# Kernel tuning notes

Measured on AMD Instinct MI355X. Metric: run time of the kernel, lower is better.

The kernel has to match this reference:

```python
import jax, jax.numpy as jnp
import numpy as np

B, V, CODE_NUM = 64, 100, 4096
CODE_SIZE, ATT, VISIT, TIME, HID, OUT = 256, 128, 256, 64, 512, 90
TYPE_NUM = 32
NEG = -2.0 ** 31


def setup_inputs() -> dict:
    key = jax.random.key(0)
    ks = jax.random.split(key, 24)
    s = 0.02
    return {
        'code_x': jax.random.randint(ks[0], (B, V, CODE_NUM), 0, 2).astype(jnp.float32),
        'code_type0': jax.random.randint(ks[1], (CODE_NUM + 1,), 0, TYPE_NUM),
        'code_type1': jax.random.randint(ks[2], (CODE_NUM + 1,), 0, TYPE_NUM),
        'code_type2': jax.random.randint(ks[3], (CODE_NUM + 1,), 0, TYPE_NUM),
        'lens': jax.random.randint(ks[4], (B,), 1, V + 1),
        'intervals': jax.random.uniform(ks[5], (B, V), dtype=jnp.float32),
        # encoder: code + 3 type embedding tables (rows 1..code_num used)
        'code_emb': jax.random.normal(ks[6], (CODE_NUM + 1, CODE_SIZE), jnp.float32) * s,
        't0_emb': jax.random.normal(ks[7], (TYPE_NUM, CODE_SIZE), jnp.float32) * s,
        't1_emb': jax.random.normal(ks[8], (TYPE_NUM, CODE_SIZE), jnp.float32) * s,
        't2_emb': jax.random.normal(ks[9], (TYPE_NUM, CODE_SIZE), jnp.float32) * s,
        # visit self-attention (no bias, per nn.Linear(..., bias=False))
        'Wq': jax.random.normal(ks[10], (CODE_SIZE, ATT), jnp.float32) * s,
        'Wk': jax.random.normal(ks[11], (CODE_SIZE, ATT), jnp.float32) * s,
        'Wv': jax.random.normal(ks[12], (CODE_SIZE, VISIT), jnp.float32) * s,
        # time embedding Linear(1, time_size)
        'time_w': jax.random.normal(ks[13], (TIME,), jnp.float32) * s,
        'time_b': jnp.zeros((TIME,), jnp.float32),
        # GRUCell params (torch layout: gates ordered r,z,n)
        'gru_Wih': jax.random.normal(ks[14], (3 * HID, VISIT + TIME), jnp.float32) * s,
        'gru_Whh': jax.random.normal(ks[15], (3 * HID, HID), jnp.float32) * s,
        'gru_bih': jnp.zeros((3 * HID,), jnp.float32),
        'gru_bhh': jnp.zeros((3 * HID,), jnp.float32),
        # classifier
        'cls_W': jax.random.normal(ks[16], (OUT, HID), jnp.float32) * s,
        'cls_b': jnp.zeros((OUT,), jnp.float32),
    }


def reference(code_x, code_type0, code_type1, code_type2, lens, intervals,
              code_emb, t0_emb, t1_emb, t2_emb, Wq, Wk, Wv, time_w, time_b,
              gru_Wih, gru_Whh, gru_bih, gru_bhh, cls_W, cls_b):
    # --- Encoder (vectorized): multi-hot slot i corresponds to code id i+1 ---
    E = (code_emb[1:]
         + t0_emb[code_type0[1:]]
         + t1_emb[code_type1[1:]]
         + t2_emb[code_type2[1:]])                      # [CODE_NUM, CODE_SIZE]
    active = (code_x > 0).astype(E.dtype)               # [B, V, CODE_NUM]
    counts = jnp.maximum(active.sum(-1, keepdims=True), 1.0)
    v_emb_ini = jnp.einsum('bvc,cd->bvd', active, E) / counts  # mean over codes
    visit_mask = jnp.arange(V)[None, :] < lens[:, None]        # [B, V]
    v_emb_ini = v_emb_ini * visit_mask[..., None]              # padded visits stay 0

    # --- Context-aware visit self-attention ---
    Q = v_emb_ini @ Wq                                   # [B, V, ATT]
    K = v_emb_ini @ Wk
    Vv = v_emb_ini @ Wv                                  # [B, V, VISIT]
    alpha = jnp.einsum('bqa,bka->bqk', Q, K)
    alpha = jnp.where(visit_mask[:, None, :], alpha, NEG)  # mask keys
    alpha = jax.nn.softmax(alpha, axis=2)
    v_emb = jnp.einsum('bqk,bkd->bqd', alpha, Vv) + Vv     # [B, V, VISIT]

    # --- Time-aware input ---
    t_emb = intervals[..., None] * time_w + time_b         # [B, V, TIME]
    x = jnp.concatenate([v_emb, t_emb], axis=-1)           # [B, V, VISIT+TIME]

    # --- GRU over visits, gated by per-patient length ---
    def step(h, xm):
        xt, mt = xm                                        # xt [B,D], mt [B]
        gi = xt @ gru_Wih.T + gru_bih
        gh = h @ gru_Whh.T + gru_bhh
        ir, iz, inn = jnp.split(gi, 3, axis=-1)
        hr, hz, hn = jnp.split(gh, 3, axis=-1)
        r = jax.nn.sigmoid(ir + hr)
        z = jax.nn.sigmoid(iz + hz)
        n = jnp.tanh(inn + r * hn)
        h_new = (1.0 - z) * n + z * h
        h = jnp.where(mt[:, None], h_new, h)
        return h, None

    h0 = jnp.zeros((B, HID), x.dtype)
    h_final, _ = jax.lax.scan(step, h0, (x.transpose(1, 0, 2), visit_mask.T))

    # --- Classifier (dropout p=0 -> identity) ---
    return jax.nn.sigmoid(h_final @ cls_W.T + cls_b)       # [B, OUT]
```

## Files before the change

kernel.cpp:

```cpp
#include <hip/hip_runtime.h>
#include <hip/hip_bf16.h>

typedef float  f32x4 __attribute__((ext_vector_type(4)));
typedef short  s16x8 __attribute__((ext_vector_type(8)));

#define NEGBIG -1e30f

__device__ __forceinline__ unsigned short f2b(float f) {
    union { float f; unsigned u; } c; c.f = f;
    unsigned r = c.u + 0x7FFF + ((c.u >> 16) & 1);
    return (unsigned short)(r >> 16);
}
__device__ __forceinline__ float b2f(unsigned short h) {
    union { unsigned u; float f; } c; c.u = ((unsigned)h) << 16;
    return c.f;
}
__device__ __forceinline__ float sigm(float x) { return 1.f / (1.f + __expf(-x)); }

__device__ __forceinline__ s16x8 ld_b128_sc(const unsigned short* p) {
    s16x8 r;
    asm volatile("global_load_dwordx4 %0, %1, off sc0 sc1" : "=v"(r) : "v"(p));
    return r;
}
__device__ __forceinline__ void st_short_sc(unsigned short* p, unsigned short v) {
    unsigned int dv = v;
    asm volatile("global_store_short %0, %1, off sc0 sc1" :: "v"(p), "v"(dv) : "memory");
}
__device__ __forceinline__ void st_dword_sc(float* p, float v) {
    asm volatile("global_store_dword %0, %1, off sc0 sc1" :: "v"(p), "v"(v) : "memory");
}

__global__ void init_zero(int* flags, unsigned short* hb0) {
    int t = threadIdx.x;
    for (int i = t; i < 1024; i += 256) flags[i] = 0;
    for (int i = t; i < 32768; i += 256) hb0[i] = 0;
}

__global__ void prep_w(const float* Wq, const float* Wk, const float* Wv,
                       const float* gWih, const float* gWhh,
                       unsigned short* wcat, unsigned short* wih, unsigned short* whh) {
    int idx = blockIdx.x * 256 + threadIdx.x;
    int stride = gridDim.x * 256;
    const int N1 = 131072, N2 = 491520, N3 = 786432;
    for (; idx < N1 + N2 + N3; idx += stride) {
        if (idx < N1) {
            int n = idx >> 8, k = idx & 255;
            float v;
            if (n < 128) v = Wq[k * 128 + n];
            else if (n < 256) v = Wk[k * 128 + (n - 128)];
            else v = Wv[k * 256 + (n - 256)];
            wcat[n * 256 + k] = f2b(v);
        } else if (idx < N1 + N2) {
            int i = idx - N1; wih[i] = f2b(gWih[i]);
        } else {
            int i = idx - N1 - N2; whh[i] = f2b(gWhh[i]);
        }
    }
}

__global__ __launch_bounds__(256) void prep_et(const float* code_emb, const int* ct0, const int* ct1, const int* ct2,
                                               const float* t0e, const float* t1e, const float* t2e,
                                               unsigned short* ET) {
    __shared__ float tile[64][65];
    const int d0 = blockIdx.x * 64, c0 = blockIdx.y * 64;
    const int t = threadIdx.x;
    for (int p = 0; p < 16; ++p) {
        int idx = p * 256 + t;
        int dl = idx & 63, cl = idx >> 6;
        int code = c0 + cl + 1;
        int d = d0 + dl;
        float v = code_emb[code * 256 + d] + t0e[ct0[code] * 256 + d]
                + t1e[ct1[code] * 256 + d] + t2e[ct2[code] * 256 + d];
        tile[dl][cl] = v;
    }
    __syncthreads();
    for (int p = 0; p < 2; ++p) {
        int idx = p * 256 + t;
        int dl = idx >> 3, ch = idx & 7;
        s16x8 pk;
#pragma unroll
        for (int e = 0; e < 8; ++e) pk[e] = (short)f2b(tile[dl][ch * 8 + e]);
        *(s16x8*)(ET + (size_t)(d0 + dl) * 4096 + c0 + ch * 8) = pk;
    }
}

__global__ __launch_bounds__(256) void enc_gemm(const float* code_x, const unsigned short* ET,
                                                const int* lens, unsigned short* Vb) {
    __shared__ __align__(16) char sm[4096 + 32768 + 128];
    char* As = sm;
    char* Bs = sm + 4096;
    float* cl = (float*)(sm + 4096 + 32768);
    const int m0 = blockIdx.x * 32;
    const int t = threadIdx.x, l = t & 63, w = t >> 6;
    const int lr = l & 15, lq = l >> 4, l7 = l & 7;
    const int sr = t >> 3, sc = t & 7;
    f32x4 acc[2][4];
#pragma unroll
    for (int a = 0; a < 2; ++a)
#pragma unroll
        for (int b = 0; b < 4; ++b) acc[a][b] = (f32x4){0.f, 0.f, 0.f, 0.f};
    int cnt = 0;
    for (int it = 0; it < 64; ++it) {
        const int k0 = it * 64;
        const float* ga = code_x + (size_t)(m0 + sr) * 4096 + k0 + sc * 8;
        f32x4 a0 = *(const f32x4*)ga;
        f32x4 a1 = *(const f32x4*)(ga + 4);
        s16x8 ap;
#pragma unroll
        for (int e = 0; e < 4; ++e) { bool on = a0[e] > 0.f; ap[e] = on ? (short)0x3F80 : (short)0; cnt += on ? 1 : 0; }
#pragma unroll
        for (int e = 0; e < 4; ++e) { bool on = a1[e] > 0.f; ap[4 + e] = on ? (short)0x3F80 : (short)0; cnt += on ? 1 : 0; }
        *(s16x8*)(As + sr * 128 + ((sc ^ (sr & 7)) << 4)) = ap;
#pragma unroll
        for (int rd = 0; rd < 8; ++rd) {
            int i = rd * 256 + t;
            int n = i >> 3, cc = i & 7;
            s16x8 bv = *(const s16x8*)(ET + (size_t)n * 4096 + k0 + cc * 8);
            *(s16x8*)(Bs + n * 128 + ((cc ^ (n & 7)) << 4)) = bv;
        }
        __syncthreads();
#pragma unroll
        for (int kk = 0; kk < 2; ++kk) {
            const int cp = kk * 4 + lq;
            s16x8 af[2], bf[4];
#pragma unroll
            for (int mt = 0; mt < 2; ++mt)
                af[mt] = *(const s16x8*)(As + (mt * 16 + lr) * 128 + ((cp ^ l7) << 4));
#pragma unroll
            for (int nt = 0; nt < 4; ++nt)
                bf[nt] = *(const s16x8*)(Bs + ((w * 4 + nt) * 16 + lr) * 128 + ((cp ^ l7) << 4));
#pragma unroll
            for (int mt = 0; mt < 2; ++mt)
#pragma unroll
                for (int nt = 0; nt < 4; ++nt)
                    acc[mt][nt] = __builtin_amdgcn_mfma_f32_16x16x32_bf16(af[mt], bf[nt], acc[mt][nt], 0, 0, 0);
        }
        __syncthreads();
    }
    float fc = (float)cnt;
    fc += __shfl_xor(fc, 1); fc += __shfl_xor(fc, 2); fc += __shfl_xor(fc, 4);
    if (sc == 0) cl[sr] = fmaxf(fc, 1.f);
    __syncthreads();
#pragma unroll
    for (int mt = 0; mt < 2; ++mt)
#pragma unroll
        for (int i = 0; i < 4; ++i) {
            int m = mt * 16 + lq * 4 + i;
            int gm = m0 + m;
            float rc = 1.f / cl[m];
            unsigned bi = (unsigned)gm / 100u;
            unsigned vi = (unsigned)gm - bi * 100u;
            float msk = ((int)vi < lens[bi]) ? 1.f : 0.f;
#pragma unroll
            for (int nt = 0; nt < 4; ++nt) {
                int n = (w * 4 + nt) * 16 + lr;
                Vb[(size_t)gm * 256 + n] = f2b(acc[mt][nt][i] * rc * msk);
            }
        }
}

__global__ __launch_bounds__(256) void gemm_bf16(const unsigned short* A, const unsigned short* Bm,
                                                 int K, int Ntot, int mode,
                                                 unsigned short* outp, const float* bias) {
    __shared__ __align__(16) char sm[4096 + 32768];
    char* As = sm;
    char* Bs = sm + 4096;
    const int m0 = blockIdx.x * 32;
    const int n0 = blockIdx.y * 256;
    const int t = threadIdx.x, l = t & 63, w = t >> 6;
    const int lr = l & 15, lq = l >> 4, l7 = l & 7;
    const int sr = t >> 3, sc = t & 7;
    const int iters = K >> 6;
    f32x4 acc[2][4];
#pragma unroll
    for (int a = 0; a < 2; ++a)
#pragma unroll
        for (int b = 0; b < 4; ++b) acc[a][b] = (f32x4){0.f, 0.f, 0.f, 0.f};
    for (int it = 0; it < iters; ++it) {
        const int k0 = it * 64;
        s16x8 av = *(const s16x8*)(A + (size_t)(m0 + sr) * K + k0 + sc * 8);
        *(s16x8*)(As + sr * 128 + ((sc ^ (sr & 7)) << 4)) = av;
#pragma unroll
        for (int rd = 0; rd < 8; ++rd) {
            int i = rd * 256 + t;
            int n = i >> 3, cc = i & 7;
            s16x8 bv = *(const s16x8*)(Bm + (size_t)(n0 + n) * K + k0 + cc * 8);
            *(s16x8*)(Bs + n * 128 + ((cc ^ (n & 7)) << 4)) = bv;
        }
        __syncthreads();
#pragma unroll
        for (int kk = 0; kk < 2; ++kk) {
            const int cp = kk * 4 + lq;
            s16x8 af[2], bf[4];
#pragma unroll
            for (int mt = 0; mt < 2; ++mt)
                af[mt] = *(const s16x8*)(As + (mt * 16 + lr) * 128 + ((cp ^ l7) << 4));
#pragma unroll
            for (int nt = 0; nt < 4; ++nt)
                bf[nt] = *(const s16x8*)(Bs + ((w * 4 + nt) * 16 + lr) * 128 + ((cp ^ l7) << 4));
#pragma unroll
            for (int mt = 0; mt < 2; ++mt)
#pragma unroll
                for (int nt = 0; nt < 4; ++nt)
                    acc[mt][nt] = __builtin_amdgcn_mfma_f32_16x16x32_bf16(af[mt], bf[nt], acc[mt][nt], 0, 0, 0);
        }
        __syncthreads();
    }
#pragma unroll
    for (int mt = 0; mt < 2; ++mt)
#pragma unroll
        for (int i = 0; i < 4; ++i) {
            int gm = m0 + mt * 16 + lq * 4 + i;
#pragma unroll
            for (int nt = 0; nt < 4; ++nt) {
                int n = n0 + (w * 4 + nt) * 16 + lr;
                float v = acc[mt][nt][i];
                if (mode == 1) v += bias[n];
                outp[(size_t)gm * Ntot + n] = f2b(v);
            }
        }
}

__global__ __launch_bounds__(256) void attn_kernel(const unsigned short* QKV, const int* lens,
                                                   const float* intervals, const float* time_w, const float* time_b,
                                                   unsigned short* X) {
    __shared__ __align__(16) char sm[28672 + 32768];
    char* Pb = sm;
    char* VTb = sm + 28672;
    const int b = blockIdx.x;
    const int t = threadIdx.x, l = t & 63, w = t >> 6;
    const int lr = l & 15, lq = l >> 4;
    const int lenb = lens[b];
    for (int p = 0; p < 7; ++p) {
        int idx = p * 256 + t;
        *(f32x4*)(Pb + idx * 16) = (f32x4){0.f, 0.f, 0.f, 0.f};
    }
    __syncthreads();
    f32x4 S[2][7];
#pragma unroll
    for (int a = 0; a < 2; ++a)
#pragma unroll
        for (int c = 0; c < 7; ++c) S[a][c] = (f32x4){0.f, 0.f, 0.f, 0.f};
#pragma unroll
    for (int kk = 0; kk < 4; ++kk) {
        s16x8 qa[2], kb[7];
#pragma unroll
        for (int mi = 0; mi < 2; ++mi) {
            int mt = 2 * w + mi;
            if (mt > 6) continue;
            int row = b * 100 + mt * 16 + lr;
            qa[mi] = *(const s16x8*)(QKV + (size_t)row * 512 + kk * 32 + lq * 8);
        }
#pragma unroll
        for (int nt = 0; nt < 7; ++nt) {
            int row = b * 100 + nt * 16 + lr;
            kb[nt] = *(const s16x8*)(QKV + (size_t)row * 512 + 128 + kk * 32 + lq * 8);
        }
#pragma unroll
        for (int mi = 0; mi < 2; ++mi) {
            int mt = 2 * w + mi;
            if (mt > 6) continue;
#pragma unroll
            for (int nt = 0; nt < 7; ++nt)
                S[mi][nt] = __builtin_amdgcn_mfma_f32_16x16x32_bf16(qa[mi], kb[nt], S[mi][nt], 0, 0, 0);
        }
    }
#pragma unroll
    for (int mi = 0; mi < 2; ++mi) {
        int mt = 2 * w + mi;
        if (mt > 6) continue;
        float sv[7][4];
#pragma unroll
        for (int nt = 0; nt < 7; ++nt) {
            int j = nt * 16 + lr;
#pragma unroll
            for (int i = 0; i < 4; ++i)
                sv[nt][i] = (j < lenb) ? S[mi][nt][i] : NEGBIG;
        }
#pragma unroll
        for (int i = 0; i < 4; ++i) {
            float mx = sv[0][i];
#pragma unroll
            for (int nt = 1; nt < 7; ++nt) mx = fmaxf(mx, sv[nt][i]);
            mx = fmaxf(mx, __shfl_xor(mx, 1));
            mx = fmaxf(mx, __shfl_xor(mx, 2));
            mx = fmaxf(mx, __shfl_xor(mx, 4));
            mx = fmaxf(mx, __shfl_xor(mx, 8));
            float e[7], sum = 0.f;
#pragma unroll
            for (int nt = 0; nt < 7; ++nt) { e[nt] = __expf(sv[nt][i] - mx); sum += e[nt]; }
            sum += __shfl_xor(sum, 1);
            sum += __shfl_xor(sum, 2);
            sum += __shfl_xor(sum, 4);
            sum += __shfl_xor(sum, 8);
            float rs = 1.f / sum;
            int m = mt * 16 + lq * 4 + i;
#pragma unroll
            for (int nt = 0; nt < 7; ++nt) {
                int j = nt * 16 + lr;
                *(unsigned short*)(Pb + m * 256 + (((j >> 3) ^ (m & 7)) << 4) + ((j & 7) << 1)) = f2b(e[nt] * rs);
            }
        }
    }
    __syncthreads();
    for (int h = 0; h < 2; ++h) {
        for (int p = 0; p < 8; ++p) {
            int idx = p * 256 + t;
            *(f32x4*)(VTb + idx * 16) = (f32x4){0.f, 0.f, 0.f, 0.f};
        }
        __syncthreads();
        for (int p = 0; p < 7; ++p) {
            int ci = p * 256 + t;
            if (ci < 1600) {
                int j = ci >> 4, d8 = ci & 15;
                s16x8 vv = *(const s16x8*)(QKV + (size_t)(b * 100 + j) * 512 + 256 + h * 128 + d8 * 8);
#pragma unroll
                for (int e = 0; e < 8; ++e) {
                    int dl = d8 * 8 + e;
                    *(unsigned short*)(VTb + dl * 256 + (((j >> 3) ^ (dl & 7)) << 4) + ((j & 7) << 1)) = (unsigned short)vv[e];
                }
            }
        }
        __syncthreads();
        f32x4 O[2][8];
#pragma unroll
        for (int a = 0; a < 2; ++a)
#pragma unroll
            for (int c = 0; c < 8; ++c) O[a][c] = (f32x4){0.f, 0.f, 0.f, 0.f};
#pragma unroll
        for (int kk = 0; kk < 4; ++kk) {
            s16x8 pa[2];
#pragma unroll
            for (int mi = 0; mi < 2; ++mi) {
                int mt = 2 * w + mi;
                if (mt > 6) continue;
                int m = mt * 16 + lr;
                pa[mi] = *(const s16x8*)(Pb + m * 256 + (((kk * 4 + lq) ^ (m & 7)) << 4));
            }
#pragma unroll
            for (int nt = 0; nt < 8; ++nt) {
                int dl = nt * 16 + lr;
                s16x8 vb = *(const s16x8*)(VTb + dl * 256 + (((kk * 4 + lq) ^ (dl & 7)) << 4));
#pragma unroll
                for (int mi = 0; mi < 2; ++mi) {
                    int mt = 2 * w + mi;
                    if (mt > 6) continue;
                    O[mi][nt] = __builtin_amdgcn_mfma_f32_16x16x32_bf16(pa[mi], vb, O[mi][nt], 0, 0, 0);
                }
            }
        }
#pragma unroll
        for (int mi = 0; mi < 2; ++mi) {
            int mt = 2 * w + mi;
            if (mt > 6) continue;
#pragma unroll
            for (int i = 0; i < 4; ++i) {
                int m = mt * 16 + lq * 4 + i;
                if (m < 100) {
#pragma unroll
                    for (int nt = 0; nt < 8; ++nt) {
                        int dl = nt * 16 + lr;
                        float res = b2f(*(unsigned short*)(VTb + dl * 256 + (((m >> 3) ^ (dl & 7)) << 4) + ((m & 7) << 1)));
                        X[(size_t)(b * 100 + m) * 320 + h * 128 + dl] = f2b(O[mi][nt][i] + res);
                    }
                }
            }
        }
        if (h == 0) __syncthreads();
    }
    for (int p = 0; p < 25; ++p) {
        int idx = p * 256 + t;
        int m = idx >> 6, d = idx & 63;
        float val = intervals[b * 100 + m] * time_w[d] + time_b[d];
        X[(size_t)(b * 100 + m) * 320 + 256 + d] = f2b(val);
    }
}

__global__ __launch_bounds__(256, 1) void gru_kernel(const unsigned short* GIb, const unsigned short* WHH,
                                                     const float* gbhh, const int* lens,
                                                     unsigned short* hb0, unsigned short* hb1, float* hf,
                                                     int* flags, const float* clsW, const float* clsb, float* out) {
    const int bid = blockIdx.x;
    const int t = threadIdx.x, l = t & 63, w = t >> 6;
    const int lr = l & 15, lq = l >> 4;
    const int d0 = bid * 16;
    const int j = d0 + lr;
    int ml;
    {
        int v = lens[l];
        v = max(v, __shfl_xor(v, 1));  v = max(v, __shfl_xor(v, 2));
        v = max(v, __shfl_xor(v, 4));  v = max(v, __shfl_xor(v, 8));
        v = max(v, __shfl_xor(v, 16)); v = max(v, __shfl_xor(v, 32));
        ml = v;
    }
    int lens4[4];
#pragma unroll
    for (int i = 0; i < 4; ++i) lens4[i] = lens[w * 16 + lq * 4 + i];
    const float bhr = gbhh[j], bhz = gbhh[512 + j], bhn = gbhh[1024 + j];
    s16x8 Bf[3][16];
#pragma unroll
    for (int g = 0; g < 3; ++g)
#pragma unroll
        for (int kk = 0; kk < 16; ++kk)
            Bf[g][kk] = *(const s16x8*)(WHH + (size_t)(g * 512 + j) * 512 + kk * 32 + lq * 8);
    float ho[4] = {0.f, 0.f, 0.f, 0.f};
    size_t gi_base[4];
#pragma unroll
    for (int i = 0; i < 4; ++i) gi_base[i] = (size_t)((w * 16 + lq * 4 + i) * 100) * 1536 + j;

    float gir[4], giz[4], gin[4];
#pragma unroll
    for (int i = 0; i < 4; ++i) {
        const unsigned short* gp = GIb + gi_base[i];
        gir[i] = b2f(gp[0]); giz[i] = b2f(gp[512]); gin[i] = b2f(gp[1024]);
    }

    for (int step = 0; step < ml; ++step) {
        const unsigned short* hb = (step & 1) ? hb1 : hb0;
        unsigned short* hn = (step & 1) ? hb0 : hb1;
        s16x8 af[16];
#pragma unroll
        for (int kk = 0; kk < 16; ++kk)
            af[kk] = ld_b128_sc(hb + (size_t)(w * 16 + lr) * 512 + kk * 32 + lq * 8);
        asm volatile("s_waitcnt vmcnt(0)" ::: "memory");
        __builtin_amdgcn_sched_barrier(0);
        f32x4 ar = (f32x4){0.f,0.f,0.f,0.f}, az = ar, an = ar;
#pragma unroll
        for (int kk = 0; kk < 16; ++kk) {
            ar = __builtin_amdgcn_mfma_f32_16x16x32_bf16(af[kk], Bf[0][kk], ar, 0, 0, 0);
            az = __builtin_amdgcn_mfma_f32_16x16x32_bf16(af[kk], Bf[1][kk], az, 0, 0, 0);
            an = __builtin_amdgcn_mfma_f32_16x16x32_bf16(af[kk], Bf[2][kk], an, 0, 0, 0);
        }
#pragma unroll
        for (int i = 0; i < 4; ++i) {
            float r = sigm(gir[i] + ar[i] + bhr);
            float z = sigm(giz[i] + az[i] + bhz);
            float n = tanhf(gin[i] + r * (an[i] + bhn));
            float hv = (step < lens4[i]) ? ((1.f - z) * n + z * ho[i]) : ho[i];
            ho[i] = hv;
            st_short_sc(hn + (size_t)(w * 16 + lq * 4 + i) * 512 + j, f2b(hv));
        }
        asm volatile("s_waitcnt vmcnt(0)" ::: "memory");
        __syncthreads();
        if (t == 0)
            __hip_atomic_store(flags + bid * 16, step + 1, __ATOMIC_RELAXED, __HIP_MEMORY_SCOPE_AGENT);
        if (step + 1 < ml) {
#pragma unroll
            for (int i = 0; i < 4; ++i) {
                const unsigned short* gp = GIb + gi_base[i] + (size_t)(step + 1) * 1536;
                gir[i] = b2f(gp[0]); giz[i] = b2f(gp[512]); gin[i] = b2f(gp[1024]);
            }
        }
        if (w == 0) {
            int guard = 0;
            while (true) {
                int v = (l < 32) ? __hip_atomic_load(flags + l * 16, __ATOMIC_RELAXED, __HIP_MEMORY_SCOPE_AGENT) : (step + 1);
                if (__all(v >= step + 1)) break;
                if (++guard > (1 << 20)) break;
                __builtin_amdgcn_s_sleep(1);
            }
        }
        __syncthreads();
    }
#pragma unroll
    for (int i = 0; i < 4; ++i)
        st_dword_sc(hf + (size_t)(w * 16 + lq * 4 + i) * 512 + j, ho[i]);
    asm volatile("s_waitcnt vmcnt(0)" ::: "memory");
    __syncthreads();
    if (t == 0)
        __hip_atomic_store(flags + bid * 16, ml + 1, __ATOMIC_RELAXED, __HIP_MEMORY_SCOPE_AGENT);
    if (w == 0) {
        int guard = 0;
        while (true) {
            int v = (l < 32) ? __hip_atomic_load(flags + l * 16, __ATOMIC_RELAXED, __HIP_MEMORY_SCOPE_AGENT) : (ml + 1);
            if (__all(v >= ml + 1)) break;
            if (++guard > (1 << 20)) break;
            __builtin_amdgcn_s_sleep(1);
        }
    }
    __syncthreads();
    if (bid < 30) {
        int bb = t >> 2, qq = t & 3;
        int c0 = bid * 3;
        float s0 = 0.f, s1 = 0.f, s2 = 0.f;
        for (int kc = 0; kc < 32; ++kc) {
            int k = qq * 128 + kc * 4;
            f32x4 hv = *(const f32x4*)(hf + bb * 512 + k);
            f32x4 w0 = *(const f32x4*)(clsW + (c0 + 0) * 512 + k);
            f32x4 w1 = *(const f32x4*)(clsW + (c0 + 1) * 512 + k);
            f32x4 w2 = *(const f32x4*)(clsW + (c0 + 2) * 512 + k);
            s0 += hv[0] * w0[0] + hv[1] * w0[1] + hv[2] * w0[2] + hv[3] * w0[3];
            s1 += hv[0] * w1[0] + hv[1] * w1[1] + hv[2] * w1[2] + hv[3] * w1[3];
            s2 += hv[0] * w2[0] + hv[1] * w2[1] + hv[2] * w2[2] + hv[3] * w2[3];
        }
        s0 += __shfl_xor(s0, 1); s0 += __shfl_xor(s0, 2);
        s1 += __shfl_xor(s1, 1); s1 += __shfl_xor(s1, 2);
        s2 += __shfl_xor(s2, 1); s2 += __shfl_xor(s2, 2);
        if (qq == 0) {
            out[bb * 90 + c0 + 0] = sigm(s0 + clsb[c0 + 0]);
            out[bb * 90 + c0 + 1] = sigm(s1 + clsb[c0 + 1]);
            out[bb * 90 + c0 + 2] = sigm(s2 + clsb[c0 + 2]);
        }
    }
}

extern "C" void kernel_launch(void* const* d_in, const int* in_sizes, int n_in,
                              void* d_out, int out_size, void* d_ws, size_t ws_size,
                              hipStream_t stream) {
    const float* code_x   = (const float*)d_in[0];
    const int*   ct0      = (const int*)d_in[1];
    const int*   ct1      = (const int*)d_in[2];
    const int*   ct2      = (const int*)d_in[3];
    const int*   lens     = (const int*)d_in[4];
    const float* intervals= (const float*)d_in[5];
    const float* code_emb = (const float*)d_in[6];
    const float* t0e      = (const float*)d_in[7];
    const float* t1e      = (const float*)d_in[8];
    const float* t2e      = (const float*)d_in[9];
    const float* Wq       = (const float*)d_in[10];
    const float* Wk       = (const float*)d_in[11];
    const float* Wv       = (const float*)d_in[12];
    const float* time_w   = (const float*)d_in[13];
    const float* time_b   = (const float*)d_in[14];
    const float* gWih     = (const float*)d_in[15];
    const float* gWhh     = (const float*)d_in[16];
    const float* gbih     = (const float*)d_in[17];
    const float* gbhh     = (const float*)d_in[18];
    const float* clsW     = (const float*)d_in[19];
    const float* clsb     = (const float*)d_in[20];

    char* ws = (char*)d_ws;
    const size_t ET_OFF   = 0;
    const size_t WCAT_OFF = 2097152;
    const size_t WIH_OFF  = 2359296;
    const size_t WHH_OFF  = 3342336;
    const size_t V_OFF    = 4915200;
    const size_t QKV_OFF  = 8192000;
    const size_t X_OFF    = 14778368;
    const size_t GI_OFF   = 18874368;
    const size_t HB0_OFF  = 38535168;
    const size_t HB1_OFF  = 38600704;
    const size_t HF_OFF   = 38666240;
    const size_t FLG_OFF  = 38797312;

    unsigned short* ET   = (unsigned short*)(ws + ET_OFF);
    unsigned short* WCAT = (unsigned short*)(ws + WCAT_OFF);
    unsigned short* WIH  = (unsigned short*)(ws + WIH_OFF);
    unsigned short* WHH  = (unsigned short*)(ws + WHH_OFF);
    unsigned short* Vb   = (unsigned short*)(ws + V_OFF);
    unsigned short* QKV  = (unsigned short*)(ws + QKV_OFF);
    unsigned short* Xb   = (unsigned short*)(ws + X_OFF);
    unsigned short* GIb  = (unsigned short*)(ws + GI_OFF);
    unsigned short* hb0  = (unsigned short*)(ws + HB0_OFF);
    unsigned short* hb1  = (unsigned short*)(ws + HB1_OFF);
    float*          hf   = (float*)(ws + HF_OFF);
    int*            flags= (int*)(ws + FLG_OFF);

    init_zero<<<1, 256, 0, stream>>>(flags, hb0);
    prep_w<<<512, 256, 0, stream>>>(Wq, Wk, Wv, gWih, gWhh, WCAT, WIH, WHH);
    prep_et<<<dim3(4, 64), 256, 0, stream>>>(code_emb, ct0, ct1, ct2, t0e, t1e, t2e, ET);
    enc_gemm<<<200, 256, 0, stream>>>(code_x, ET, lens, Vb);
    gemm_bf16<<<dim3(200, 2), 256, 0, stream>>>(Vb, WCAT, 256, 512, 2, QKV, nullptr);
    attn_kernel<<<64, 256, 0, stream>>>(QKV, lens, intervals, time_w, time_b, Xb);
    gemm_bf16<<<dim3(200, 6), 256, 0, stream>>>(Xb, WIH, 320, 1536, 1, GIb, gbih);
    gru_kernel<<<32, 256, 0, stream>>>(GIb, WHH, gbhh, lens, hb0, hb1, hf, flags, clsW, clsb, (float*)d_out);
}
```

Measured before the change: 769.9 us.

## Replace GRU flag barrier with sentinel-polled triple-buffered hidden state

Replaces the per-step grid-wide flag barrier in the persistent GRU kernel with data-driven synchronization. Hidden-state buffers are pre-filled with a 0xFFFF bf16 sentinel, and each wave polls its own A-fragment loads until no sentinel remains. Three buffers rotate so the next-next buffer can be reset while the current one is consumed. This removes the __syncthreads, flag stores and spin loops from each step, but depends on 0xFFFF (a NaN pattern) never being a real value and on the ordering of the sentinel resets.

After: 858.4 us. +11.5%, slower.

```diff
diff --git a/kernel.cpp b/kernel.cpp
--- a/kernel.cpp
+++ b/kernel.cpp
@@ -26,14 +26,38 @@
     unsigned int dv = v;
     asm volatile("global_store_short %0, %1, off sc0 sc1" :: "v"(p), "v"(dv) : "memory");
 }
-__device__ __forceinline__ void st_dword_sc(float* p, float v) {
-    asm volatile("global_store_dword %0, %1, off sc0 sc1" :: "v"(p), "v"(v) : "memory");
-}
-
-__global__ void init_zero(int* flags, unsigned short* hb0) {
-    int t = threadIdx.x;
-    for (int i = t; i < 1024; i += 256) flags[i] = 0;
-    for (int i = t; i < 32768; i += 256) hb0[i] = 0;
+
+#define POLL_H(BASE, AF) do {                                                        \
+    unsigned okm_ = 0; int guard_ = 0;                                               \
+    while (true) {                                                                   \
+        _Pragma("unroll")                                                            \
+        for (int kk_ = 0; kk_ < 16; ++kk_)                                           \
+            if (!((okm_ >> kk_) & 1)) AF[kk_] = ld_b128_sc((BASE) + kk_ * 32);       \
+        asm volatile("s_waitcnt vmcnt(0)" ::: "memory");                             \
+        __builtin_amdgcn_sched_barrier(0);                                           \
+        _Pragma("unroll")                                                            \
+        for (int kk_ = 0; kk_ < 16; ++kk_) if (!((okm_ >> kk_) & 1)) {               \
+            bool bad_ = false;                                                       \
+            _Pragma("unroll")                                                        \
+            for (int e_ = 0; e_ < 8; ++e_)                                           \
+                bad_ = bad_ || ((unsigned short)AF[kk_][e_] == (unsigned short)0xFFFFu); \
+            if (!bad_) okm_ |= (1u << kk_);                                          \
+        }                                                                            \
+        if (__all(okm_ == 0xFFFFu)) break;                                           \
+        if (++guard_ > (1 << 18)) break;                        \
+    }                                                                                \
+    __builtin_amdgcn_sched_barrier(0);                                               \
+} while (0)
+
+__global__ void init_zero(int* flags, unsigned short* hb0, unsigned short* hb1, unsigned short* hb2) {
+    int idx = blockIdx.x * 256 + threadIdx.x;
+    int stride = gridDim.x * 256;
+    for (int i = idx; i < 1024; i += stride) flags[i] = 0;
+    for (int i = idx; i < 32768; i += stride) {
+        hb0[i] = 0;
+        hb1[i] = 0xFFFFu;
+        hb2[i] = 0xFFFFu;
+    }
 }
 
 __global__ void prep_w(const float* Wq, const float* Wk, const float* Wv,
@@ -378,13 +402,12 @@
 
 __global__ __launch_bounds__(256, 1) void gru_kernel(const unsigned short* GIb, const unsigned short* WHH,
                                                      const float* gbhh, const int* lens,
-                                                     unsigned short* hb0, unsigned short* hb1, float* hf,
-                                                     int* flags, const float* clsW, const float* clsb, float* out) {
+                                                     unsigned short* hbA, unsigned short* hbB, unsigned short* hbC,
+                                                     const float* clsW, const float* clsb, float* out) {
     const int bid = blockIdx.x;
     const int t = threadIdx.x, l = t & 63, w = t >> 6;
     const int lr = l & 15, lq = l >> 4;
-    const int d0 = bid * 16;
-    const int j = d0 + lr;
+    const int j = bid * 16 + lr;
     int ml;
     {
         int v = lens[l];
@@ -405,8 +428,13 @@
             Bf[g][kk] = *(const s16x8*)(WHH + (size_t)(g * 512 + j) * 512 + kk * 32 + lq * 8);
     float ho[4] = {0.f, 0.f, 0.f, 0.f};
     size_t gi_base[4];
-#pragma unroll
-    for (int i = 0; i < 4; ++i) gi_base[i] = (size_t)((w * 16 + lq * 4 + i) * 100) * 1536 + j;
+    size_t hrow[4];
+#pragma unroll
+    for (int i = 0; i < 4; ++i) {
+        gi_base[i] = (size_t)((w * 16 + lq * 4 + i) * 100) * 1536 + j;
+        hrow[i]    = (size_t)(w * 16 + lq * 4 + i) * 512 + j;
+    }
+    const size_t arow = (size_t)(w * 16 + lr) * 512 + lq * 8;
 
     float gir[4], giz[4], gin[4];
 #pragma unroll
@@ -415,15 +443,15 @@
         gir[i] = b2f(gp[0]); giz[i] = b2f(gp[512]); gin[i] = b2f(gp[1024]);
     }
 
+    unsigned short* rb = hbA;
+    unsigned short* wb = hbB;
+    unsigned short* pb = hbC;
+
     for (int step = 0; step < ml; ++step) {
-        const unsigned short* hb = (step & 1) ? hb1 : hb0;
-        unsigned short* hn = (step & 1) ? hb0 : hb1;
         s16x8 af[16];
-#pragma unroll
-        for (int kk = 0; kk < 16; ++kk)
-            af[kk] = ld_b128_sc(hb + (size_t)(w * 16 + lr) * 512 + kk * 32 + lq * 8);
-        asm volatile("s_waitcnt vmcnt(0)" ::: "memory");
-        __builtin_amdgcn_sched_barrier(0);
+        POLL_H(rb + arow, af);
+#pragma unroll
+        for (int i = 0; i < 4; ++i) st_short_sc(pb + hrow[i], (unsigned short)0xFFFFu);
         f32x4 ar = (f32x4){0.f,0.f,0.f,0.f}, az = ar, an = ar;
 #pragma unroll
         for (int kk = 0; kk < 16; ++kk) {
@@ -438,12 +466,8 @@
             float n = tanhf(gin[i] + r * (an[i] + bhn));
             float hv = (step < lens4[i]) ? ((1.f - z) * n + z * ho[i]) : ho[i];
             ho[i] = hv;
-            st_short_sc(hn + (size_t)(w * 16 + lq * 4 + i) * 512 + j, f2b(hv));
-        }
-        asm volatile("s_waitcnt vmcnt(0)" ::: "memory");
-        __syncthreads();
-        if (t == 0)
-            __hip_atomic_store(flags + bid * 16, step + 1, __ATOMIC_RELAXED, __HIP_MEMORY_SCOPE_AGENT);
+            st_short_sc(wb + hrow[i], f2b(hv));
+        }
         if (step + 1 < ml) {
 #pragma unroll
             for (int i = 0; i < 4; ++i) {
@@ -451,47 +475,35 @@
                 gir[i] = b2f(gp[0]); giz[i] = b2f(gp[512]); gin[i] = b2f(gp[1024]);
             }
         }
-        if (w == 0) {
-            int guard = 0;
-            while (true) {
-                int v = (l < 32) ? __hip_atomic_load(flags + l * 16, __ATOMIC_RELAXED, __HIP_MEMORY_SCOPE_AGENT) : (step + 1);
-                if (__all(v >= step + 1)) break;
-                if (++guard > (1 << 20)) break;
-                __builtin_amdgcn_s_sleep(1);
-            }
-        }
-        __syncthreads();
-    }
-#pragma unroll
-    for (int i = 0; i < 4; ++i)
-        st_dword_sc(hf + (size_t)(w * 16 + lq * 4 + i) * 512 + j, ho[i]);
-    asm volatile("s_waitcnt vmcnt(0)" ::: "memory");
-    __syncthreads();
-    if (t == 0)
-        __hip_atomic_store(flags + bid * 16, ml + 1, __ATOMIC_RELAXED, __HIP_MEMORY_SCOPE_AGENT);
-    if (w == 0) {
-        int guard = 0;
-        while (true) {
-            int v = (l < 32) ? __hip_atomic_load(flags + l * 16, __ATOMIC_RELAXED, __HIP_MEMORY_SCOPE_AGENT) : (ml + 1);
-            if (__all(v >= ml + 1)) break;
-            if (++guard > (1 << 20)) break;
-            __builtin_amdgcn_s_sleep(1);
-        }
-    }
-    __syncthreads();
+        unsigned short* tmp = rb; rb = wb; wb = pb; pb = tmp;
+    }
+
     if (bid < 30) {
+        {
+            s16x8 af[16];
+            POLL_H(rb + arow, af);
+        }
+        const unsigned short* fbuf = rb;
         int bb = t >> 2, qq = t & 3;
         int c0 = bid * 3;
         float s0 = 0.f, s1 = 0.f, s2 = 0.f;
-        for (int kc = 0; kc < 32; ++kc) {
-            int k = qq * 128 + kc * 4;
-            f32x4 hv = *(const f32x4*)(hf + bb * 512 + k);
-            f32x4 w0 = *(const f32x4*)(clsW + (c0 + 0) * 512 + k);
-            f32x4 w1 = *(const f32x4*)(clsW + (c0 + 1) * 512 + k);
-            f32x4 w2 = *(const f32x4*)(clsW + (c0 + 2) * 512 + k);
-            s0 += hv[0] * w0[0] + hv[1] * w0[1] + hv[2] * w0[2] + hv[3] * w0[3];
-            s1 += hv[0] * w1[0] + hv[1] * w1[1] + hv[2] * w1[2] + hv[3] * w1[3];
-            s2 += hv[0] * w2[0] + hv[1] * w2[1] + hv[2] * w2[2] + hv[3] * w2[3];
+        for (int kc = 0; kc < 16; ++kc) {
+            int k = qq * 128 + kc * 8;
+            s16x8 hvb = *(const s16x8*)(fbuf + (size_t)bb * 512 + k);
+            f32x4 w0a = *(const f32x4*)(clsW + (size_t)(c0 + 0) * 512 + k);
+            f32x4 w0b = *(const f32x4*)(clsW + (size_t)(c0 + 0) * 512 + k + 4);
+            f32x4 w1a = *(const f32x4*)(clsW + (size_t)(c0 + 1) * 512 + k);
+            f32x4 w1b = *(const f32x4*)(clsW + (size_t)(c0 + 1) * 512 + k + 4);
+            f32x4 w2a = *(const f32x4*)(clsW + (size_t)(c0 + 2) * 512 + k);
+            f32x4 w2b = *(const f32x4*)(clsW + (size_t)(c0 + 2) * 512 + k + 4);
+#pragma unroll
+            for (int e = 0; e < 4; ++e) {
+                float h0 = b2f((unsigned short)hvb[e]);
+                float h1 = b2f((unsigned short)hvb[4 + e]);
+                s0 += h0 * w0a[e] + h1 * w0b[e];
+                s1 += h0 * w1a[e] + h1 * w1b[e];
+                s2 += h0 * w2a[e] + h1 * w2b[e];
+            }
         }
         s0 += __shfl_xor(s0, 1); s0 += __shfl_xor(s0, 2);
         s1 += __shfl_xor(s1, 1); s1 += __shfl_xor(s1, 2);
@@ -540,7 +552,7 @@
     const size_t GI_OFF   = 18874368;
     const size_t HB0_OFF  = 38535168;
     const size_t HB1_OFF  = 38600704;
-    const size_t HF_OFF   = 38666240;
+    const size_t HB2_OFF  = 38666240;
     const size_t FLG_OFF  = 38797312;
 
     unsigned short* ET   = (unsigned short*)(ws + ET_OFF);
@@ -553,15 +565,15 @@
     unsigned short* GIb  = (unsigned short*)(ws + GI_OFF);
     unsigned short* hb0  = (unsigned short*)(ws + HB0_OFF);
     unsigned short* hb1  = (unsigned short*)(ws + HB1_OFF);
-    float*          hf   = (float*)(ws + HF_OFF);
+    unsigned short* hb2  = (unsigned short*)(ws + HB2_OFF);
     int*            flags= (int*)(ws + FLG_OFF);
 
-    init_zero<<<1, 256, 0, stream>>>(flags, hb0);
+    init_zero<<<8, 256, 0, stream>>>(flags, hb0, hb1, hb2);
     prep_w<<<512, 256, 0, stream>>>(Wq, Wk, Wv, gWih, gWhh, WCAT, WIH, WHH);
     prep_et<<<dim3(4, 64), 256, 0, stream>>>(code_emb, ct0, ct1, ct2, t0e, t1e, t2e, ET);
     enc_gemm<<<200, 256, 0, stream>>>(code_x, ET, lens, Vb);
     gemm_bf16<<<dim3(200, 2), 256, 0, stream>>>(Vb, WCAT, 256, 512, 2, QKV, nullptr);
     attn_kernel<<<64, 256, 0, stream>>>(QKV, lens, intervals, time_w, time_b, Xb);
     gemm_bf16<<<dim3(200, 6), 256, 0, stream>>>(Xb, WIH, 320, 1536, 1, GIb, gbih);
-    gru_kernel<<<32, 256, 0, stream>>>(GIb, WHH, gbhh, lens, hb0, hb1, hf, flags, clsW, clsb, (float*)d_out);
-}
+    gru_kernel<<<32, 256, 0, stream>>>(GIb, WHH, gbhh, lens, hb0, hb1, hb2, clsW, clsb, (float*)d_out);
+}
```
